# Kernel optimization log

Measured on AMD Instinct MI355X. Metric: run time of the kernel, lower is better.

Reference implementation:

```python
import jax, jax.numpy as jnp
import numpy as np

NUM_WIRES = 14
N_LAYERS = 4
BATCH = 128


def _rx_mat(theta):
    # PennyLane RX(t) = [[cos(t/2), -i sin(t/2)], [-i sin(t/2), cos(t/2)]]
    c = jnp.cos(theta / 2).astype(jnp.complex64)
    s = jnp.sin(theta / 2).astype(jnp.complex64)
    row0 = jnp.stack([c, -1j * s], axis=-1)
    row1 = jnp.stack([-1j * s, c], axis=-1)
    return jnp.stack([row0, row1], axis=-2)  # (..., 2, 2)


def _rz_mat(theta):
    # PennyLane RZ(t) = diag(exp(-it/2), exp(it/2))
    e0 = jnp.exp(-1j * theta.astype(jnp.complex64) / 2)
    e1 = jnp.exp(1j * theta.astype(jnp.complex64) / 2)
    z = jnp.zeros_like(e0)
    row0 = jnp.stack([e0, z], axis=-1)
    row1 = jnp.stack([z, e1], axis=-1)
    return jnp.stack([row0, row1], axis=-2)


def _apply_1q(psi, gate, wire):
    # psi: (B, 2, 2, ..., 2); gate: (2,2) shared or (B,2,2) per-sample
    axis = wire + 1
    psi = jnp.moveaxis(psi, axis, -1)
    if gate.ndim == 2:
        psi = psi @ gate.T
    else:
        psi = jnp.einsum('b...j,bij->b...i', psi, gate)
    return jnp.moveaxis(psi, -1, axis)


def _apply_cnot(psi, ctrl, tgt):
    ac, at = ctrl + 1, tgt + 1
    psi0 = jnp.take(psi, 0, axis=ac)
    psi1 = jnp.take(psi, 1, axis=ac)
    at_adj = at - (1 if at > ac else 0)  # target axis shifts after removing ctrl axis
    psi1 = jnp.flip(psi1, axis=at_adj)   # X on target when ctrl=1
    return jnp.stack([psi0, psi1], axis=ac)


def _circuit(x, weights):
    # x: (B, n) real angles; weights: (L, n, 2)
    B = x.shape[0]
    n = NUM_WIRES
    psi = jnp.zeros((B,) + (2,) * n, jnp.complex64)
    psi = psi.at[(slice(None),) + (0,) * n].set(1.0)  # |0...0>
    # data encoding: per-sample RX gates
    for i in range(n):
        psi = _apply_1q(psi, _rx_mat(x[:, i]), i)
    # variational ansatz
    for l in range(N_LAYERS):
        for i in range(n):
            psi = _apply_1q(psi, _rx_mat(weights[l, i, 0]), i)
            psi = _apply_1q(psi, _rz_mat(weights[l, i, 1]), i)
        for i in range(n - 1):
            psi = _apply_cnot(psi, i, i + 1)
        psi = _apply_cnot(psi, n - 1, 0)
    # <Z_i> for every wire
    p = jnp.abs(psi) ** 2  # (B, 2, ..., 2) real
    zs = []
    for i in range(n):
        other = tuple(a for a in range(1, n + 1) if a != i + 1)
        m = jnp.sum(p, axis=other)  # (B, 2)
        zs.append(m[:, 0] - m[:, 1])
    return jnp.stack(zs, axis=-1)  # (B, n)


def setup_inputs() -> dict:
    key = jax.random.key(0)
    k1, k2, k3, k4 = jax.random.split(key, 4)
    states = jax.random.normal(k1, (BATCH, 2 ** NUM_WIRES), dtype=jnp.float32)
    weights = jax.random.normal(k2, (N_LAYERS, NUM_WIRES, 2), dtype=jnp.float32)
    lim = 1.0 / np.sqrt(NUM_WIRES)
    head_w = jax.random.uniform(k3, (1, NUM_WIRES), jnp.float32, -lim, lim)
    head_b = jax.random.uniform(k4, (1,), jnp.float32, -lim, lim)
    return {"states": states, "weights": weights, "head_w": head_w, "head_b": head_b}


def reference(states, weights, head_w, head_b):
    features = jnp.abs(states)[:, :NUM_WIRES]        # (B, n)
    qfeatures = _circuit(features, weights)          # (B, n)
    out = (qfeatures @ head_w.T + head_b)[:, 0]      # (B,)
    return out
```

## Files before the change

kernel.cpp:

```cpp
#include <hip/hip_runtime.h>
#include <math.h>

#define NW 14
#define NSTATE 16384
#define HALF 8192
#define NL 4
#define BATCH 128
#define TPB 1024
#define SHB1 (84 * 1024)
#define SHB2 ((NSTATE + 3 * TPB) * (int)sizeof(float2))


#define B4_  0x201Fu
#define B5_  0x203Fu
#define B12_ 0x3FFFu
#define B13_ 0x1FFFu

#define WAVE_FENCE() __builtin_amdgcn_wave_barrier()

__device__ __forceinline__ unsigned sxmap(unsigned v) {
    unsigned t = v;
    t ^= t >> 1; t ^= t >> 2; t ^= t >> 4; t ^= t >> 8;
    return (t & 0x0FFFu) | ((t & 1u) << 13);
}

__device__ __forceinline__ float2 cmul(float2 u, float2 v) {
    return make_float2(u.x * v.x - u.y * v.y, u.x * v.y + u.y * v.x);
}

__device__ __forceinline__ float4 fused_coef(const float* weights,
                                             const float* states,
                                             int b, int l, int w) {
    float t1 = weights[(l * NW + w) * 2 + 0];
    float t2 = weights[(l * NW + w) * 2 + 1];
    if (l == 0) t1 += fabsf(states[(size_t)b * NSTATE + w]);
    float s, c, sz, cz;
    sincosf(0.5f * t1, &s, &c);
    sincosf(0.5f * t2, &sz, &cz);
    return make_float4(c * cz, -c * sz, -s * sz, -s * cz);
}

template<int N, int M>
__device__ __forceinline__ void gateN(float2* r, float4 g, unsigned s3) {
    const float f = (s3 & (unsigned)M) ? -1.0f : 1.0f;
    g.y *= f;
    g.z *= f;
#pragma unroll
    for (int k = 0; k < N; ++k) {
        if ((k & M) == 0) {
            const float x0 = r[k].x,   y0 = r[k].y;
            const float x1 = r[k|M].x, y1 = r[k|M].y;
            r[k].x   =  g.x*x0 - g.y*y0 + g.z*x1 - g.w*y1;
            r[k].y   =  g.x*y0 + g.y*x0 + g.z*y1 + g.w*x1;
            r[k|M].x = -g.z*x0 - g.w*y0 + g.x*x1 + g.y*y1;
            r[k|M].y = -g.z*y0 + g.w*x0 + g.x*y1 - g.y*x1;
        }
    }
}

template<int J0, int S3SH, int S3MSK>
__device__ __forceinline__ void pass3h(float2* psi, const float4* gc,
                                       unsigned t) {
    const float4 gA = gc[13 - (J0 + 0)];
    const float4 gB = gc[13 - (J0 + 1)];
    const float4 gC = gc[13 - (J0 + 2)];
    const unsigned s3   = (t >> S3SH) & (unsigned)S3MSK;
    const unsigned low  = t & ((1u << J0) - 1u);
    const unsigned high = (t >> J0) << (J0 + 3);
    float2 r[8];
#pragma unroll
    for (int k = 0; k < 8; ++k)
        r[k] = psi[low | (((unsigned)k ^ s3) << J0) | high];
    gateN<8,1>(r, gA, s3);
    gateN<8,2>(r, gB, s3);
    gateN<8,4>(r, gC, s3);
#pragma unroll
    for (int k = 0; k < 8; ++k)
        psi[low | (((unsigned)k ^ s3) << J0) | high] = r[k];
}

template<int J0, int S3SH, int S3MSK>
__device__ __forceinline__ void pass3f(float2* psi, const float4* gc,
                                       unsigned t) {
    const float4 gA = gc[13 - (J0 + 0)];
    const float4 gB = gc[13 - (J0 + 1)];
    const float4 gC = gc[13 - (J0 + 2)];
    const unsigned s3 = (t >> S3SH) & (unsigned)S3MSK;
#pragma unroll
    for (int m = 0; m < 2; ++m) {
        const unsigned x    = t | ((unsigned)m << 10);
        const unsigned low  = x & ((1u << J0) - 1u);
        const unsigned high = (x >> J0) << (J0 + 3);
        float2 r[8];
#pragma unroll
        for (int k = 0; k < 8; ++k)
            r[k] = psi[low | (((unsigned)k ^ s3) << J0) | high];
        gateN<8,1>(r, gA, s3);
        gateN<8,2>(r, gB, s3);
        gateN<8,4>(r, gC, s3);
#pragma unroll
        for (int k = 0; k < 8; ++k)
            psi[low | (((unsigned)k ^ s3) << J0) | high] = r[k];
    }
}

__device__ __forceinline__ void passE(float2* psi, float2* spare,
                                      const float4* gc4, int l, unsigned t) {
    const float4 g1 = gc4[l*NW + 1];
    const float4 g0 = gc4[l*NW + 0];

    unsigned v = t;
    v ^= v >> 1; v ^= v >> 2; v ^= v >> 4; v ^= v >> 8;
    const unsigned Rinv0 = (v & 0x0FFFu) | ((v & 1u) << 13);

    float2 c0[4];
#pragma unroll
    for (int k = 0; k < 4; ++k) c0[k] = psi[t | ((unsigned)k << 12)];
    gateN<4,1>(c0, g1, 0u);
    gateN<4,2>(c0, g0, 0u);
    spare[3*t+0] = c0[1];
    spare[3*t+1] = c0[2];
    spare[3*t+2] = c0[3];
    const float2 keep = c0[0];

    float2 r[12];
#pragma unroll
    for (int m = 1; m < 4; ++m) {
        const unsigned base = t | ((unsigned)m << 10);
#pragma unroll
        for (int k = 0; k < 4; ++k)
            r[(m-1)*4 + k] = psi[base | ((unsigned)k << 12)];
    }
#pragma unroll
    for (int m = 0; m < 3; ++m) {
        gateN<4,1>(r + 4*m, g1, 0u);
        gateN<4,2>(r + 4*m, g0, 0u);
    }

    __syncthreads();

#pragma unroll
    for (int m = 1; m < 4; ++m) {
        const unsigned Rb = Rinv0 ^ ((m & 1) ? 0x27FFu : 0u)
                                  ^ ((m & 2) ? 0x2FFFu : 0u);
#pragma unroll
        for (int k = 0; k < 4; ++k) {
            const unsigned CK = ((k & 1) ? B12_ : 0u) ^ ((k & 2) ? B13_ : 0u);
            psi[Rb ^ CK] = r[(m-1)*4 + k];
        }
    }
    psi[Rinv0]           = keep;
    psi[Rinv0 ^ B12_]    = spare[3*t+0];
    psi[Rinv0 ^ B13_]    = spare[3*t+1];
    psi[Rinv0 ^ 0x2000u] = spare[3*t+2];
}

__device__ __forceinline__ void exit_scatter(const float2* psi,
                                             float2* __restrict__ dst,
                                             float4 g1, unsigned q,
                                             unsigned tid) {
#pragma unroll
    for (int m = 0; m < 4; ++m) {
        const unsigned jc = tid + (unsigned)m * TPB;
        const float2 x0 = psi[jc];
        const float2 x1 = psi[jc | 0x1000u];
        float2 A0, A1;
        A0.x =  g1.x*x0.x - g1.y*x0.y + g1.z*x1.x - g1.w*x1.y;
        A0.y =  g1.x*x0.y + g1.y*x0.x + g1.z*x1.y + g1.w*x1.x;
        A1.x = -g1.z*x0.x - g1.w*x0.y + g1.x*x1.x + g1.y*x1.y;
        A1.y = -g1.z*x0.y + g1.w*x0.x + g1.x*x1.y - g1.y*x1.x;
        const unsigned d0 = sxmap(jc) ^ (q ? 0x1FFFu : 0u);
        dst[d0]           = A0;
        dst[d0 ^ 0x3FFFu] = A1;
    }
}

__global__ __launch_bounds__(TPB) void k_layer1(
    const float* __restrict__ states, const float* __restrict__ weights,
    float2* __restrict__ Sout)
{
    extern __shared__ float2 psi[];
    __shared__ float2 vfac[NW][2];
    __shared__ float2 T1[128];
    __shared__ float2 T2[128];
    __shared__ float4 gc[NW];
    const unsigned gid = blockIdx.x, q = gid >> 7, b = gid & 127u;
    const unsigned tid = threadIdx.x;

    if (tid < NW) {
        float4 g = fused_coef(weights, states, (int)b, 0, (int)tid);
        vfac[tid][0] = make_float2(g.x, g.y);
        vfac[tid][1] = make_float2(-g.z, g.w);
    }
    if (tid >= 64 && tid < 64 + NW)
        gc[tid - 64] = fused_coef(weights, states, (int)b, 1, (int)(tid - 64));
    __syncthreads();
    if (tid < 128) {
        float2 p = make_float2(1.0f, 0.0f);
#pragma unroll
        for (int j = 0; j < 7; ++j)
            p = cmul(p, vfac[13 - j][(tid >> j) & 1u]);
        T1[tid] = p;
    } else if (tid < 256) {
        const unsigned u = tid - 128;
        float2 p = make_float2(1.0f, 0.0f);
#pragma unroll
        for (int j = 7; j < 14; ++j)
            p = cmul(p, vfac[13 - j][(u >> (j - 7)) & 1u]);
        T2[u] = p;
    }
    __syncthreads();

#pragma unroll
    for (int m = 0; m < 8; ++m) {
        const unsigned I  = tid + (unsigned)m * TPB;
        const unsigned If = I | (q << 13);
        const unsigned lo  = (If ^ (If >> 1)) & 0x0FFFu;
        const unsigned y12 = ((If >> 12) ^ (If >> 13) ^ If) & 1u;
        const unsigned y13 = ((If >> 13) ^ If) & 1u;
        const unsigned J = lo | (y12 << 12) | (y13 << 13);
        psi[I] = cmul(T1[J & 127u], T2[J >> 7]);
    }
    __syncthreads();

    pass3h<0, 1, 7>(psi, gc, tid);  WAVE_FENCE();
    pass3h<3, 3, 1>(psi, gc, tid);  WAVE_FENCE();
    pass3h<6, 0, 0>(psi, gc, tid);  __syncthreads();
    pass3h<9, 0, 0>(psi, gc, tid);  __syncthreads();

    exit_scatter(psi, Sout + (size_t)b * NSTATE, gc[1], q, tid);
}

__global__ __launch_bounds__(TPB) void k_rest(
    const float* __restrict__ states, const float* __restrict__ weights,
    const float* __restrict__ head_w, const float* __restrict__ head_b,
    const float2* __restrict__ Sin, float* __restrict__ out)
{
    extern __shared__ float2 dyn[];
    float2* psi   = dyn;
    float2* spare = dyn + NSTATE;
    __shared__ float4 gc4[NL * NW];
    __shared__ float wsum[TPB / 64];
    const unsigned b = blockIdx.x;
    const unsigned tid = threadIdx.x;

    if (tid < NL * NW)
        gc4[tid] = fused_coef(weights, states, (int)b,
                              (int)tid / NW, (int)tid % NW);
    __syncthreads();

    {
        const float4 ge = gc4[1 * NW + 0];
#pragma unroll
        for (int qm = 0; qm < 8; ++qm) {
            const unsigned q = (unsigned)qm >> 2;
            const unsigned m = (unsigned)qm & 3u;
            const float2* src = Sin + (size_t)b * NSTATE + (size_t)q * HALF;
            const unsigned ic = tid + m * TPB;
            const float2 f0 = src[ic];
            const float2 f1 = src[ic ^ 0x1FFFu];
            const unsigned rc = (q ^ ic) & 1u;
            const float aar = ge.x, aai = rc ? -ge.y : ge.y;
            const float bbr = rc ? -ge.z : ge.z, bbi = ge.w;
            float2 oc, op;
            oc.x = aar*f0.x - aai*f0.y + bbr*f1.x - bbi*f1.y;
            oc.y = aar*f0.y + aai*f0.x + bbr*f1.y + bbi*f1.x;
            op.x = aar*f1.x + aai*f1.y - (bbr*f0.x + bbi*f0.y);
            op.y = aar*f1.y - aai*f1.x - (bbr*f0.y - bbi*f0.x);
            psi[(q << 13) | ic]            = oc;
            psi[(q << 13) | (ic ^ 0x1FFFu)] = op;
        }
    }
    __syncthreads();

    pass3f<0, 1, 7>(psi, gc4 + 2 * NW, tid);  WAVE_FENCE();
    pass3f<3, 3, 1>(psi, gc4 + 2 * NW, tid);  WAVE_FENCE();
    pass3f<6, 0, 0>(psi, gc4 + 2 * NW, tid);  __syncthreads();
    pass3f<9, 0, 0>(psi, gc4 + 2 * NW, tid);  __syncthreads();
    passE(psi, spare, gc4, 2, tid);           __syncthreads();

    pass3f<0, 1, 7>(psi, gc4 + 3 * NW, tid);  WAVE_FENCE();
    pass3f<3, 3, 1>(psi, gc4 + 3 * NW, tid);  WAVE_FENCE();
    pass3f<6, 0, 0>(psi, gc4 + 3 * NW, tid);  __syncthreads();
    pass3f<9, 0, 0>(psi, gc4 + 3 * NW, tid);  __syncthreads();

    float hw[NW];
#pragma unroll
    for (int i = 0; i < NW; ++i) hw[i] = head_w[i];
    float H = 0.0f, H12 = 0.0f;
#pragma unroll
    for (int i = 0; i < NW; ++i) H += hw[i];
#pragma unroll
    for (int i = 2; i < NW; ++i) H12 += hw[i];

    const float4 g1 = gc4[3 * NW + 1];
    const float4 g0 = gc4[3 * NW + 0];

    float acc = 0.0f;
#pragma unroll
    for (int m2 = 0; m2 < 4; ++m2) {
        const unsigned base = tid | ((unsigned)m2 << 10);
        float2 r[4];
#pragma unroll
        for (int k = 0; k < 4; ++k)
            r[k] = psi[base | ((unsigned)k << 12)];
        gateN<4,1>(r, g1, 0u);
        gateN<4,2>(r, g0, 0u);
        float A = 0.0f;
        unsigned sfx = 0u;
#pragma unroll
        for (int p = 11; p >= 0; --p) {
            sfx ^= (base >> p) & 1u;
            if (sfx) A += hw[13 - p];
        }
        const unsigned P = sfx;
#pragma unroll
        for (int k = 0; k < 4; ++k) {
            const unsigned u   = ((unsigned)k ^ ((unsigned)k >> 1)) & 1u;
            const unsigned b13 = P ^ ((unsigned)k & 1u);
            float sum = u ? (H12 - A) : A;
            if (u)   sum += hw[1];
            if (b13) sum += hw[0];
            const float cv = H - 2.0f * sum;
            acc += (r[k].x * r[k].x + r[k].y * r[k].y) * cv;
        }
    }
#pragma unroll
    for (int off = 32; off > 0; off >>= 1)
        acc += __shfl_down(acc, off, 64);
    if ((tid & 63u) == 0) wsum[tid >> 6] = acc;
    __syncthreads();
    if (tid == 0) {
        float tot = 0.0f;
#pragma unroll
        for (int i = 0; i < TPB / 64; ++i) tot += wsum[i];
        out[b] = tot + head_b[0];
    }
}

extern "C" void kernel_launch(void* const* d_in, const int* in_sizes, int n_in,
                              void* d_out, int out_size, void* d_ws, size_t ws_size,
                              hipStream_t stream) {
    const float* states  = (const float*)d_in[0];
    const float* weights = (const float*)d_in[1];
    const float* head_w  = (const float*)d_in[2];
    const float* head_b  = (const float*)d_in[3];
    float* out = (float*)d_out;

    float2* SA = (float2*)d_ws;

    k_layer1<<<2 * BATCH, TPB, SHB1, stream>>>(states, weights, SA);
    k_rest  <<<BATCH, TPB, SHB2, stream>>>(states, weights, head_w, head_b,
                                           SA, out);
}
```

Baseline: 102.0 us.

## Split remaining layers into half-state kernels over 2x batch blocks

Replaces the single k_rest kernel, which held the full 16384-amplitude state per block, with two kernels, k_mid and k_last. Each runs 256 blocks that each own half the state, reusing the half-state pass3h and exit_scatter path from layer 1. The final kernel folds the wire-0 gate into the load, and the halves' partial expectations are combined with atomicAdd after k_mid writes the bias. The aim is better occupancy and parallelism, lower shared memory per block and removal of passE's spare buffer, at the cost of an extra kernel launch and a global-memory round trip of the state through a second workspace buffer.

```diff
diff --git a/kernel.cpp b/kernel.cpp
--- a/kernel.cpp
+++ b/kernel.cpp
@@ -8,11 +8,8 @@
 #define BATCH 128
 #define TPB 1024
 #define SHB1 (84 * 1024)
-#define SHB2 ((NSTATE + 3 * TPB) * (int)sizeof(float2))
-
-
-#define B4_  0x201Fu
-#define B5_  0x203Fu
+
+
 #define B12_ 0x3FFFu
 #define B13_ 0x1FFFu
 
@@ -77,82 +74,6 @@
 #pragma unroll
     for (int k = 0; k < 8; ++k)
         psi[low | (((unsigned)k ^ s3) << J0) | high] = r[k];
-}
-
-template<int J0, int S3SH, int S3MSK>
-__device__ __forceinline__ void pass3f(float2* psi, const float4* gc,
-                                       unsigned t) {
-    const float4 gA = gc[13 - (J0 + 0)];
-    const float4 gB = gc[13 - (J0 + 1)];
-    const float4 gC = gc[13 - (J0 + 2)];
-    const unsigned s3 = (t >> S3SH) & (unsigned)S3MSK;
-#pragma unroll
-    for (int m = 0; m < 2; ++m) {
-        const unsigned x    = t | ((unsigned)m << 10);
-        const unsigned low  = x & ((1u << J0) - 1u);
-        const unsigned high = (x >> J0) << (J0 + 3);
-        float2 r[8];
-#pragma unroll
-        for (int k = 0; k < 8; ++k)
-            r[k] = psi[low | (((unsigned)k ^ s3) << J0) | high];
-        gateN<8,1>(r, gA, s3);
-        gateN<8,2>(r, gB, s3);
-        gateN<8,4>(r, gC, s3);
-#pragma unroll
-        for (int k = 0; k < 8; ++k)
-            psi[low | (((unsigned)k ^ s3) << J0) | high] = r[k];
-    }
-}
-
-__device__ __forceinline__ void passE(float2* psi, float2* spare,
-                                      const float4* gc4, int l, unsigned t) {
-    const float4 g1 = gc4[l*NW + 1];
-    const float4 g0 = gc4[l*NW + 0];
-
-    unsigned v = t;
-    v ^= v >> 1; v ^= v >> 2; v ^= v >> 4; v ^= v >> 8;
-    const unsigned Rinv0 = (v & 0x0FFFu) | ((v & 1u) << 13);
-
-    float2 c0[4];
-#pragma unroll
-    for (int k = 0; k < 4; ++k) c0[k] = psi[t | ((unsigned)k << 12)];
-    gateN<4,1>(c0, g1, 0u);
-    gateN<4,2>(c0, g0, 0u);
-    spare[3*t+0] = c0[1];
-    spare[3*t+1] = c0[2];
-    spare[3*t+2] = c0[3];
-    const float2 keep = c0[0];
-
-    float2 r[12];
-#pragma unroll
-    for (int m = 1; m < 4; ++m) {
-        const unsigned base = t | ((unsigned)m << 10);
-#pragma unroll
-        for (int k = 0; k < 4; ++k)
-            r[(m-1)*4 + k] = psi[base | ((unsigned)k << 12)];
-    }
-#pragma unroll
-    for (int m = 0; m < 3; ++m) {
-        gateN<4,1>(r + 4*m, g1, 0u);
-        gateN<4,2>(r + 4*m, g0, 0u);
-    }
-
-    __syncthreads();
-
-#pragma unroll
-    for (int m = 1; m < 4; ++m) {
-        const unsigned Rb = Rinv0 ^ ((m & 1) ? 0x27FFu : 0u)
-                                  ^ ((m & 2) ? 0x2FFFu : 0u);
-#pragma unroll
-        for (int k = 0; k < 4; ++k) {
-            const unsigned CK = ((k & 1) ? B12_ : 0u) ^ ((k & 2) ? B13_ : 0u);
-            psi[Rb ^ CK] = r[(m-1)*4 + k];
-        }
-    }
-    psi[Rinv0]           = keep;
-    psi[Rinv0 ^ B12_]    = spare[3*t+0];
-    psi[Rinv0 ^ B13_]    = spare[3*t+1];
-    psi[Rinv0 ^ 0x2000u] = spare[3*t+2];
 }
 
 __device__ __forceinline__ void exit_scatter(const float2* psi,
@@ -231,32 +152,28 @@
     exit_scatter(psi, Sout + (size_t)b * NSTATE, gc[1], q, tid);
 }
 
-__global__ __launch_bounds__(TPB) void k_rest(
+__global__ __launch_bounds__(TPB) void k_mid(
     const float* __restrict__ states, const float* __restrict__ weights,
-    const float* __restrict__ head_w, const float* __restrict__ head_b,
-    const float2* __restrict__ Sin, float* __restrict__ out)
+    const float* __restrict__ head_b,
+    const float2* __restrict__ Sin, float2* __restrict__ Sout,
+    float* __restrict__ out)
 {
-    extern __shared__ float2 dyn[];
-    float2* psi   = dyn;
-    float2* spare = dyn + NSTATE;
-    __shared__ float4 gc4[NL * NW];
-    __shared__ float wsum[TPB / 64];
-    const unsigned b = blockIdx.x;
+    extern __shared__ float2 psi[];
+    __shared__ float4 gcx[NW + 1];
+    const unsigned gid = blockIdx.x, q = gid >> 7, b = gid & 127u;
     const unsigned tid = threadIdx.x;
 
-    if (tid < NL * NW)
-        gc4[tid] = fused_coef(weights, states, (int)b,
-                              (int)tid / NW, (int)tid % NW);
+    if (tid < NW) gcx[tid] = fused_coef(weights, states, (int)b, 2, (int)tid);
+    if (tid == 64) gcx[NW] = fused_coef(weights, states, (int)b, 1, 0);
+    if (q == 0 && tid == 96) out[b] = head_b[0];
     __syncthreads();
 
     {
-        const float4 ge = gc4[1 * NW + 0];
-#pragma unroll
-        for (int qm = 0; qm < 8; ++qm) {
-            const unsigned q = (unsigned)qm >> 2;
-            const unsigned m = (unsigned)qm & 3u;
-            const float2* src = Sin + (size_t)b * NSTATE + (size_t)q * HALF;
-            const unsigned ic = tid + m * TPB;
+        const float4 ge = gcx[NW];
+        const float2* src = Sin + (size_t)b * NSTATE + (size_t)q * HALF;
+#pragma unroll
+        for (int m = 0; m < 4; ++m) {
+            const unsigned ic = tid + (unsigned)m * TPB;
             const float2 f0 = src[ic];
             const float2 f1 = src[ic ^ 0x1FFFu];
             const unsigned rc = (q ^ ic) & 1u;
@@ -267,22 +184,84 @@
             oc.y = aar*f0.y + aai*f0.x + bbr*f1.y + bbi*f1.x;
             op.x = aar*f1.x + aai*f1.y - (bbr*f0.x + bbi*f0.y);
             op.y = aar*f1.y - aai*f1.x - (bbr*f0.y - bbi*f0.x);
-            psi[(q << 13) | ic]            = oc;
-            psi[(q << 13) | (ic ^ 0x1FFFu)] = op;
-        }
-    }
-    __syncthreads();
-
-    pass3f<0, 1, 7>(psi, gc4 + 2 * NW, tid);  WAVE_FENCE();
-    pass3f<3, 3, 1>(psi, gc4 + 2 * NW, tid);  WAVE_FENCE();
-    pass3f<6, 0, 0>(psi, gc4 + 2 * NW, tid);  __syncthreads();
-    pass3f<9, 0, 0>(psi, gc4 + 2 * NW, tid);  __syncthreads();
-    passE(psi, spare, gc4, 2, tid);           __syncthreads();
-
-    pass3f<0, 1, 7>(psi, gc4 + 3 * NW, tid);  WAVE_FENCE();
-    pass3f<3, 3, 1>(psi, gc4 + 3 * NW, tid);  WAVE_FENCE();
-    pass3f<6, 0, 0>(psi, gc4 + 3 * NW, tid);  __syncthreads();
-    pass3f<9, 0, 0>(psi, gc4 + 3 * NW, tid);  __syncthreads();
+            psi[ic]           = oc;
+            psi[ic ^ 0x1FFFu] = op;
+        }
+    }
+    __syncthreads();
+
+    pass3h<0, 1, 7>(psi, gcx, tid);  WAVE_FENCE();
+    pass3h<3, 3, 1>(psi, gcx, tid);  WAVE_FENCE();
+    pass3h<6, 0, 0>(psi, gcx, tid);  __syncthreads();
+    pass3h<9, 0, 0>(psi, gcx, tid);  __syncthreads();
+
+    exit_scatter(psi, Sout + (size_t)b * NSTATE, gcx[1], q, tid);
+}
+
+__global__ __launch_bounds__(TPB) void k_last(
+    const float* __restrict__ states, const float* __restrict__ weights,
+    const float* __restrict__ head_w,
+    const float2* __restrict__ Sin, float* __restrict__ out)
+{
+    extern __shared__ float2 psi[];
+    __shared__ float4 gcx[NW + 1];
+    __shared__ float wsum[TPB / 64];
+    const unsigned gid = blockIdx.x, h = gid >> 7, b = gid & 127u;
+    const unsigned tid = threadIdx.x;
+
+    if (tid < NW) gcx[tid] = fused_coef(weights, states, (int)b, 3, (int)tid);
+    if (tid == 64) gcx[NW] = fused_coef(weights, states, (int)b, 2, 0);
+    __syncthreads();
+
+    {
+        const float4 ge = gcx[NW];
+        const float4 g0 = gcx[0];
+        const float ar = h ? -g0.z : g0.x;
+        const float ai = h ?  g0.w : g0.y;
+        const float br = h ?  g0.x : g0.z;
+        const float bi = h ? -g0.y : g0.w;
+        const float2* s0 = Sin + (size_t)b * NSTATE;
+        const float2* s1 = s0 + HALF;
+#pragma unroll
+        for (int m = 0; m < 4; ++m) {
+            const unsigned ic = tid + (unsigned)m * TPB;
+            const unsigned jc = ic ^ 0x1FFFu;
+            const float2 f00 = s0[ic], f01 = s0[jc];
+            const float2 f10 = s1[ic], f11 = s1[jc];
+            const unsigned rc = ic & 1u;
+            float2 oc0, op0, oc1, op1;
+            {
+                const float aar = ge.x, aai = rc ? -ge.y : ge.y;
+                const float bbr = rc ? -ge.z : ge.z, bbi = ge.w;
+                oc0.x = aar*f00.x - aai*f00.y + bbr*f01.x - bbi*f01.y;
+                oc0.y = aar*f00.y + aai*f00.x + bbr*f01.y + bbi*f01.x;
+                op0.x = aar*f01.x + aai*f01.y - (bbr*f00.x + bbi*f00.y);
+                op0.y = aar*f01.y - aai*f01.x - (bbr*f00.y - bbi*f00.x);
+            }
+            {
+                const unsigned rx = rc ^ 1u;
+                const float aar = ge.x, aai = rx ? -ge.y : ge.y;
+                const float bbr = rx ? -ge.z : ge.z, bbi = ge.w;
+                oc1.x = aar*f10.x - aai*f10.y + bbr*f11.x - bbi*f11.y;
+                oc1.y = aar*f10.y + aai*f10.x + bbr*f11.y + bbi*f11.x;
+                op1.x = aar*f11.x + aai*f11.y - (bbr*f10.x + bbi*f10.y);
+                op1.y = aar*f11.y - aai*f11.x - (bbr*f10.y - bbi*f10.x);
+            }
+            float2 oA, oB;
+            oA.x = ar*oc0.x - ai*oc0.y + br*oc1.x - bi*oc1.y;
+            oA.y = ar*oc0.y + ai*oc0.x + br*oc1.y + bi*oc1.x;
+            oB.x = ar*op0.x - ai*op0.y + br*op1.x - bi*op1.y;
+            oB.y = ar*op0.y + ai*op0.x + br*op1.y + bi*op1.x;
+            psi[ic] = oA;
+            psi[jc] = oB;
+        }
+    }
+    __syncthreads();
+
+    pass3h<0, 1, 7>(psi, gcx, tid);  WAVE_FENCE();
+    pass3h<3, 3, 1>(psi, gcx, tid);  WAVE_FENCE();
+    pass3h<6, 0, 0>(psi, gcx, tid);  __syncthreads();
+    pass3h<9, 0, 0>(psi, gcx, tid);  __syncthreads();
 
     float hw[NW];
 #pragma unroll
@@ -293,19 +272,15 @@
 #pragma unroll
     for (int i = 2; i < NW; ++i) H12 += hw[i];
 
-    const float4 g1 = gc4[3 * NW + 1];
-    const float4 g0 = gc4[3 * NW + 0];
-
+    const float4 g1 = gcx[1];
     float acc = 0.0f;
 #pragma unroll
     for (int m2 = 0; m2 < 4; ++m2) {
         const unsigned base = tid | ((unsigned)m2 << 10);
-        float2 r[4];
-#pragma unroll
-        for (int k = 0; k < 4; ++k)
-            r[k] = psi[base | ((unsigned)k << 12)];
-        gateN<4,1>(r, g1, 0u);
-        gateN<4,2>(r, g0, 0u);
+        float2 r[2];
+        r[0] = psi[base];
+        r[1] = psi[base | 0x1000u];
+        gateN<2,1>(r, g1, 0u);
         float A = 0.0f;
         unsigned sfx = 0u;
 #pragma unroll
@@ -315,14 +290,14 @@
         }
         const unsigned P = sfx;
 #pragma unroll
-        for (int k = 0; k < 4; ++k) {
-            const unsigned u   = ((unsigned)k ^ ((unsigned)k >> 1)) & 1u;
-            const unsigned b13 = P ^ ((unsigned)k & 1u);
+        for (int kk = 0; kk < 2; ++kk) {
+            const unsigned u   = (unsigned)kk ^ h;
+            const unsigned b13 = P ^ (unsigned)kk;
             float sum = u ? (H12 - A) : A;
             if (u)   sum += hw[1];
             if (b13) sum += hw[0];
             const float cv = H - 2.0f * sum;
-            acc += (r[k].x * r[k].x + r[k].y * r[k].y) * cv;
+            acc += (r[kk].x * r[kk].x + r[kk].y * r[kk].y) * cv;
         }
     }
 #pragma unroll
@@ -334,7 +309,7 @@
         float tot = 0.0f;
 #pragma unroll
         for (int i = 0; i < TPB / 64; ++i) tot += wsum[i];
-        out[b] = tot + head_b[0];
+        atomicAdd(out + b, tot);
     }
 }
 
@@ -348,8 +323,11 @@
     float* out = (float*)d_out;
 
     float2* SA = (float2*)d_ws;
+    float2* SB = SA + (size_t)BATCH * NSTATE;
 
     k_layer1<<<2 * BATCH, TPB, SHB1, stream>>>(states, weights, SA);
-    k_rest  <<<BATCH, TPB, SHB2, stream>>>(states, weights, head_w, head_b,
-                                           SA, out);
-}
+    k_mid   <<<2 * BATCH, TPB, SHB1, stream>>>(states, weights, head_b,
+                                               SA, SB, out);
+    k_last  <<<2 * BATCH, TPB, SHB1, stream>>>(states, weights, head_w,
+                                               SB, out);
+}
```

Measured after the change: 108.1 us. 5.9% more time.
